# Performance work log

Hardware: AMD Instinct MI355X
Metric: run time of the kernel (lower is better)

Reference implementation:

```python
import jax, jax.numpy as jnp
import numpy as np

NHID = 512
PROJ = 64          # fixed 64-dim projection from the source code
N_NODES = 16384
N_CLAIM = 4096
N_EVID = 8192
N_GRAPHS = 64


def setup_inputs() -> dict:
    key = jax.random.key(0)
    ks = jax.random.split(key, 10)
    x = jax.random.normal(ks[0], (N_NODES, NHID), dtype=jnp.float32)
    batch = jnp.sort(jax.random.randint(ks[1], (N_NODES,), 0, N_GRAPHS, dtype=jnp.int64))
    claim_index = jax.random.randint(ks[2], (N_CLAIM,), 0, N_NODES, dtype=jnp.int64)
    evidence_index = jax.random.randint(ks[3], (N_EVID,), 0, N_NODES, dtype=jnp.int64)
    # Linear params (PyTorch Linear: y = x @ W.T + b; store as [in, out] here)
    s_c = 1.0 / np.sqrt(NHID)
    Wc = jax.random.uniform(ks[4], (NHID, PROJ), jnp.float32, -s_c, s_c)
    bc = jax.random.uniform(ks[5], (PROJ,), jnp.float32, -s_c, s_c)
    We = jax.random.uniform(ks[6], (NHID, PROJ), jnp.float32, -s_c, s_c)
    be = jax.random.uniform(ks[7], (PROJ,), jnp.float32, -s_c, s_c)
    s_a = 1.0 / np.sqrt(4 * NHID)
    Wa = jax.random.uniform(ks[8], (4 * NHID, NHID), jnp.float32, -s_a, s_a)
    ba = jax.random.uniform(ks[9], (NHID,), jnp.float32, -s_a, s_a)
    return {"x": x, "batch": batch, "claim_index": claim_index,
            "evidence_index": evidence_index,
            "Wc": Wc, "bc": bc, "We": We, "be": be, "Wa": Wa, "ba": ba}


def reference(x, batch, claim_index, evidence_index, Wc, bc, We, be, Wa, ba):
    claim_batch = batch[claim_index]          # [Nc]
    evidence_batch = batch[evidence_index]    # [Ne]
    # block-diagonal mask: 0 where same graph, -inf otherwise
    same = claim_batch[:, None] == evidence_batch[None, :]
    mask = jnp.where(same, 0.0, -jnp.inf).astype(jnp.float32)  # [Nc, Ne]

    claim = x[claim_index]       # [Nc, nhid]
    evidence = x[evidence_index]  # [Ne, nhid]

    weight_c = claim @ Wc + bc    # [Nc, 64]
    weight_e = evidence @ We + be  # [Ne, 64]
    scores = weight_c @ weight_e.T + mask          # [Nc, Ne]
    attn = jax.nn.softmax(scores, axis=-1)
    claim_new = attn @ evidence                    # [Nc, nhid]

    a = jnp.concatenate([claim, claim_new, claim - claim_new, claim * claim_new], axis=-1)
    a = a @ Wa + ba               # [Nc, nhid]

    # global_mean_pool over claim_batch
    seg_sum = jax.ops.segment_sum(a, claim_batch, num_segments=N_GRAPHS)
    counts = jax.ops.segment_sum(jnp.ones((a.shape[0],), a.dtype), claim_batch,
                                 num_segments=N_GRAPHS)
    res = seg_sum / jnp.maximum(counts, 1.0)[:, None]  # [B, nhid]
    return res
```

## Files before the change

### kernel.cpp

```cpp
#include <hip/hip_runtime.h>
#include <hip/hip_bf16.h>

#define NHID 512
#define PROJ 64
#define NC 4096
#define NEV 8192
#define NG 64
#define NCMAX 128
#define NE_CAP 256
#define DSLICES 4
#define DW 128
#define WE_S_STRIDE 72
#define EV_STRIDE 264
#define PG_STRIDE 256

typedef __attribute__((ext_vector_type(8))) short s16x8;
typedef __attribute__((ext_vector_type(8))) unsigned short u16x8;
typedef __attribute__((ext_vector_type(4))) float f32x4;

static __device__ __forceinline__ unsigned short f2b(float f) {
  union { __hip_bfloat16 h; unsigned short u; } v;
  v.h = __float2bfloat16(f);
  return v.u;
}

template <int NPT>
__device__ __forceinline__ void compact_pairs(
    const int* __restrict__ batch, const int* __restrict__ idx, int g,
    int* __restrict__ off_out, int* __restrict__ cnt_out, int2* __restrict__ pairs) {
  __shared__ int wtot[4], wless[4];
  int t = threadIdx.x, lane = t & 63, w = t >> 6;
  int vals[NPT], nid[NPT];
  int base_i = t * NPT;
  int eq = 0, less = 0;
#pragma unroll
  for (int j = 0; j < NPT; j++) {
    int node = idx[base_i + j];
    int v = batch[node];
    vals[j] = v;
    nid[j] = node;
    eq += (v == g) ? 1 : 0;
    less += (v < g) ? 1 : 0;
  }
  int s = eq;
#pragma unroll
  for (int off = 1; off < 64; off <<= 1) {
    int o = __shfl_up(s, off);
    if (lane >= off) s += o;
  }
  int ls = less;
#pragma unroll
  for (int off = 32; off; off >>= 1) ls += __shfl_xor(ls, off);
  if (lane == 63) wtot[w] = s;
  if (lane == 0) wless[w] = ls;
  __syncthreads();
  int wbase = 0;
#pragma unroll
  for (int k = 0; k < 4; k++)
    if (k < w) wbase += wtot[k];
  int base = wless[0] + wless[1] + wless[2] + wless[3];
  int pos = base + wbase + (s - eq);
#pragma unroll
  for (int j = 0; j < NPT; j++) {
    if (vals[j] == g) pairs[pos++] = make_int2(base_i + j, nid[j]);
  }
  if (t == 255) {
    cnt_out[g] = wbase + s;
    off_out[g] = base;
  }
}

__global__ __launch_bounds__(256) void k_front(
    const float* __restrict__ Wc, const float* __restrict__ We,
    unsigned short* __restrict__ WcT, unsigned short* __restrict__ WeT,
    const int* __restrict__ batch, const int* __restrict__ cidx,
    const int* __restrict__ eidx, int* __restrict__ c_off, int* __restrict__ c_cnt,
    int2* __restrict__ c_pair, int* __restrict__ e_off, int* __restrict__ e_cnt,
    int2* __restrict__ e_pair) {
  int b = blockIdx.x;
  if (b < 16) {
    __shared__ float ts[64][65];
    const float* src = (b < 8) ? Wc : We;
    unsigned short* dst = (b < 8) ? WcT : WeT;
    int k0 = (b & 7) * 64;
    int t = threadIdx.x;
    int c = t & 63, r0 = t >> 6;
#pragma unroll
    for (int p = 0; p < 16; p++) {
      int r = r0 * 16 + p;
      ts[r][c] = src[(size_t)(k0 + r) * 64 + c];
    }
    __syncthreads();
    int n = t >> 2, q = t & 3;
    unsigned short tmp[16];
#pragma unroll
    for (int j = 0; j < 16; j++) tmp[j] = f2b(ts[q * 16 + j][n]);
    u16x8* dp = (u16x8*)(dst + (size_t)n * NHID + k0 + q * 16);
    dp[0] = *(u16x8*)tmp;
    dp[1] = *(u16x8*)(tmp + 8);
  } else if (b < 80) {
    compact_pairs<NC / 256>(batch, cidx, b - 16, c_off, c_cnt, c_pair);
  } else {
    compact_pairs<NEV / 256>(batch, eidx, b - 80, e_off, e_cnt, e_pair);
  }
}

__global__ __launch_bounds__(256) void k_proj(
    const float* __restrict__ x, const int* __restrict__ cidx,
    const int* __restrict__ eidx, const unsigned short* __restrict__ WcT,
    const unsigned short* __restrict__ WeT, const float* __restrict__ bc,
    const float* __restrict__ be, const float* __restrict__ Wa,
    unsigned short* __restrict__ WaT, unsigned short* __restrict__ wcp,
    unsigned short* __restrict__ wep) {
  __shared__ __align__(16) char sm[64 * 65 * 4];
  int b = blockIdx.x;
  int t = threadIdx.x;
  if (b >= 768) {
    int tb = b - 768;
    float(*ts)[65] = (float(*)[65])sm;
    int k0 = (tb >> 3) * 64, n0 = (tb & 7) * 64;
    int c = t & 63, r0 = t >> 6;
#pragma unroll
    for (int p = 0; p < 16; p++) {
      int r = r0 * 16 + p;
      ts[r][c] = Wa[(size_t)(k0 + r) * NHID + n0 + c];
    }
    __syncthreads();
    int n = t >> 2, q = t & 3;
    unsigned short tmp[16];
#pragma unroll
    for (int j = 0; j < 16; j++) tmp[j] = f2b(ts[q * 16 + j][n]);
    u16x8* dp = (u16x8*)(WaT + (size_t)(n0 + n) * (4 * NHID) + k0 + q * 16);
    dp[0] = *(u16x8*)tmp;
    dp[1] = *(u16x8*)(tmp + 8);
    return;
  }
  float(*red)[16][64] = (float(*)[16][64])sm;
  const int* idx; const unsigned short* WT; const float* bias;
  unsigned short* out; int base;
  if (b < NC / 16) { idx = cidx; WT = WcT; bias = bc; out = wcp; base = b * 16; }
  else             { idx = eidx; WT = WeT; bias = be; out = wep; base = (b - NC / 16) * 16; }
  int lane = t & 63, kh = t >> 6;
  int ln = lane & 15, kb = lane >> 4;
  const float* xr = x + (size_t)idx[base + ln] * NHID + kh * 128;
  const unsigned short* wb = WT + kh * 128;
  f32x4 acc[4];
#pragma unroll
  for (int nt = 0; nt < 4; nt++) acc[nt] = (f32x4){0.f, 0.f, 0.f, 0.f};
#pragma unroll
  for (int kt = 0; kt < 4; kt++) {
    int k0 = kt * 32 + kb * 8;
    float4 p0 = *(const float4*)(xr + k0);
    float4 p1 = *(const float4*)(xr + k0 + 4);
    s16x8 a;
    a[0] = (short)f2b(p0.x); a[1] = (short)f2b(p0.y);
    a[2] = (short)f2b(p0.z); a[3] = (short)f2b(p0.w);
    a[4] = (short)f2b(p1.x); a[5] = (short)f2b(p1.y);
    a[6] = (short)f2b(p1.z); a[7] = (short)f2b(p1.w);
#pragma unroll
    for (int nt = 0; nt < 4; nt++) {
      s16x8 bf = *(const s16x8*)(wb + (size_t)(nt * 16 + ln) * NHID + k0);
      acc[nt] = __builtin_amdgcn_mfma_f32_16x16x32_bf16(a, bf, acc[nt], 0, 0, 0);
    }
  }
#pragma unroll
  for (int nt = 0; nt < 4; nt++)
#pragma unroll
    for (int r = 0; r < 4; r++)
      red[kh][kb * 4 + r][nt * 16 + ln] = acc[nt][r];
  __syncthreads();
  for (int i = t; i < 512; i += 256) {
    int row = i >> 5, cp = i & 31;
    int c0 = cp * 2;
    float v0 = red[0][row][c0] + red[1][row][c0] + red[2][row][c0] + red[3][row][c0] + bias[c0];
    float v1 = red[0][row][c0 + 1] + red[1][row][c0 + 1] + red[2][row][c0 + 1] + red[3][row][c0 + 1] + bias[c0 + 1];
    unsigned int pk = (unsigned)f2b(v0) | ((unsigned)f2b(v1) << 16);
    *(unsigned int*)(out + (size_t)(base + row) * PROJ + c0) = pk;
  }
}

__global__ __launch_bounds__(512) void k_score(
    const unsigned short* __restrict__ wcp, const unsigned short* __restrict__ wep,
    const int* __restrict__ c_off, const int* __restrict__ c_cnt,
    const int2* __restrict__ c_pair, const int* __restrict__ e_off,
    const int* __restrict__ e_cnt, const int2* __restrict__ e_pair,
    unsigned short* __restrict__ P_g) {
  __shared__ __align__(16) unsigned short we_s[NE_CAP * WE_S_STRIDE];
  __shared__ __align__(16) unsigned short wc_s[NCMAX * WE_S_STRIDE];
  int g = blockIdx.x;
  int t = threadIdx.x, lane = t & 63, w = t >> 6;
  int ln = lane & 15, kb = lane >> 4;
  int ne = min(e_cnt[g], NE_CAP);
  int eoff = e_off[g];
  int nloc = min(c_cnt[g], NCMAX);
  int coff = c_off[g];
  if (nloc <= 0) return;
  int KT = (ne + 31) >> 5;
  int NT = KT * 2;
  {
    int q = t & 7, er = t >> 3;
    for (int base_ = 0; base_ < NE_CAP; base_ += 64) {
      int e = base_ + er;
      u16x8 v = (u16x8){0, 0, 0, 0, 0, 0, 0, 0};
      if (e < ne) v = *(const u16x8*)(wep + (size_t)e_pair[eoff + e].x * PROJ + q * 8);
      *(u16x8*)(we_s + e * WE_S_STRIDE + q * 8) = v;
    }
    for (int base_ = 0; base_ < NCMAX; base_ += 64) {
      int c = base_ + er;
      u16x8 v = (u16x8){0, 0, 0, 0, 0, 0, 0, 0};
      if (c < nloc) v = *(const u16x8*)(wcp + (size_t)c_pair[coff + c].x * PROJ + q * 8);
      *(u16x8*)(wc_s + c * WE_S_STRIDE + q * 8) = v;
    }
  }
  __syncthreads();
  f32x4 sa[16];
#pragma unroll
  for (int i = 0; i < 16; i++) sa[i] = (f32x4){0.f, 0.f, 0.f, 0.f};
  const unsigned short* arow = wc_s + ((w << 4) + ln) * WE_S_STRIDE;
#pragma unroll
  for (int ks = 0; ks < 2; ks++) {
    s16x8 af = *(const s16x8*)(arow + ks * 32 + kb * 8);
#pragma unroll
    for (int nt = 0; nt < 16; nt++) {
      if (nt < NT) {
        s16x8 bf = *(const s16x8*)(we_s + (nt * 16 + ln) * WE_S_STRIDE + ks * 32 + kb * 8);
        sa[nt] = __builtin_amdgcn_mfma_f32_16x16x32_bf16(af, bf, sa[nt], 0, 0, 0);
      }
    }
  }
#pragma unroll
  for (int r = 0; r < 4; r++) {
    int claim = (w << 4) + (kb << 2) + r;
    float mx = -1e30f;
#pragma unroll
    for (int nt = 0; nt < 16; nt++) {
      if (nt < NT) {
        float v = sa[nt][r];
        v = (nt * 16 + ln < ne) ? v : -1e30f;
        sa[nt][r] = v;
        mx = fmaxf(mx, v);
      }
    }
    mx = fmaxf(mx, __shfl_xor(mx, 1));
    mx = fmaxf(mx, __shfl_xor(mx, 2));
    mx = fmaxf(mx, __shfl_xor(mx, 4));
    mx = fmaxf(mx, __shfl_xor(mx, 8));
    float sum = 0.f;
#pragma unroll
    for (int nt = 0; nt < 16; nt++) {
      if (nt < NT) {
        float p = __expf(sa[nt][r] - mx);
        sa[nt][r] = p;
        sum += p;
      }
    }
    sum += __shfl_xor(sum, 1);
    sum += __shfl_xor(sum, 2);
    sum += __shfl_xor(sum, 4);
    sum += __shfl_xor(sum, 8);
    float inv = 1.f / sum;
    if (claim < nloc) {
      unsigned short* prow = P_g + (size_t)(coff + claim) * PG_STRIDE;
#pragma unroll
      for (int nt = 0; nt < 16; nt++) {
        if (nt < NT) prow[nt * 16 + ln] = f2b(sa[nt][r] * inv);
      }
    }
  }
}

__global__ __launch_bounds__(512, 4) void k_pv(
    const float* __restrict__ x, const unsigned short* __restrict__ P_g,
    const int* __restrict__ c_off, const int* __restrict__ c_cnt,
    const int2* __restrict__ c_pair, const int* __restrict__ e_off,
    const int* __restrict__ e_cnt, const int2* __restrict__ e_pair,
    unsigned short* __restrict__ mcb) {
  __shared__ __align__(16) unsigned short evT[DW * EV_STRIDE];
  __shared__ float pp[4][3][DW];
  __shared__ int ev_id[NE_CAP];
  __shared__ int cl_id[NCMAX];
  unsigned int* evT32 = (unsigned int*)evT;

  int g = blockIdx.x >> 2;
  int ds = blockIdx.x & 3;
  int dsbase = ds * DW;
  int t = threadIdx.x, lane = t & 63, w = t >> 6;
  int ln = lane & 15, kb = lane >> 4;

  int ne = min(e_cnt[g], NE_CAP);
  int eoff = e_off[g];
  int ccnt_full = c_cnt[g];
  int nloc = min(ccnt_full, NCMAX);
  int coff = c_off[g];
  if (nloc <= 0) {
    int q = t >> 7, d = t & 127;
    mcb[(size_t)g * 4 * NHID + q * NHID + dsbase + d] = 0;
    return;
  }
  int KT = (ne + 31) >> 5;

  for (int e = t; e < NE_CAP; e += 512)
    ev_id[e] = (e < ne) ? e_pair[eoff + e].y : 0;
  if (t < NCMAX) cl_id[t] = (t < nloc) ? c_pair[coff + t].y : 0;
  __syncthreads();

#pragma unroll
  for (int it = 0; it < 8; it++) {
    int idx2 = it * 512 + t;
    int ep = idx2 & 127;
    int dq = idx2 >> 7;
    int d0 = dq * 4;
    int e0 = ep * 2;
    float4 va = make_float4(0.f, 0.f, 0.f, 0.f);
    float4 vb = make_float4(0.f, 0.f, 0.f, 0.f);
    if (e0 < ne)     va = *(const float4*)(x + (size_t)ev_id[e0] * NHID + dsbase + d0);
    if (e0 + 1 < ne) vb = *(const float4*)(x + (size_t)ev_id[e0 + 1] * NHID + dsbase + d0);
    evT32[(d0 + 0) * (EV_STRIDE / 2) + ep] = (unsigned)f2b(va.x) | ((unsigned)f2b(vb.x) << 16);
    evT32[(d0 + 1) * (EV_STRIDE / 2) + ep] = (unsigned)f2b(va.y) | ((unsigned)f2b(vb.y) << 16);
    evT32[(d0 + 2) * (EV_STRIDE / 2) + ep] = (unsigned)f2b(va.z) | ((unsigned)f2b(vb.z) << 16);
    evT32[(d0 + 3) * (EV_STRIDE / 2) + ep] = (unsigned)f2b(va.w) | ((unsigned)f2b(vb.w) << 16);
  }
  __syncthreads();

  int mw = w >> 1, nw = w & 1;
  int m0 = mw * 32, n0 = nw * 64;
  f32x4 pc[8];
#pragma unroll
  for (int i = 0; i < 8; i++) pc[i] = (f32x4){0.f, 0.f, 0.f, 0.f};
  {
    const unsigned short* prow0 = P_g + (size_t)(coff + m0 + ln) * PG_STRIDE + kb * 8;
    const unsigned short* prow1 = prow0 + 16 * PG_STRIDE;
#pragma unroll
    for (int kt = 0; kt < 8; kt++) {
      if (kt < KT) {
        int k0 = kt * 32;
        s16x8 a0 = *(const s16x8*)(prow0 + k0);
        s16x8 a1 = *(const s16x8*)(prow1 + k0);
#pragma unroll
        for (int nt = 0; nt < 4; nt++) {
          s16x8 bf = *(const s16x8*)(evT + (n0 + nt * 16 + ln) * EV_STRIDE + k0 + kb * 8);
          pc[nt]     = __builtin_amdgcn_mfma_f32_16x16x32_bf16(a0, bf, pc[nt], 0, 0, 0);
          pc[4 + nt] = __builtin_amdgcn_mfma_f32_16x16x32_bf16(a1, bf, pc[4 + nt], 0, 0, 0);
        }
      }
    }
  }

#pragma unroll
  for (int nt = 0; nt < 4; nt++) {
    int d = n0 + nt * 16 + ln;
    float s_cl = 0.f, s_cn = 0.f, s_pr = 0.f;
#pragma unroll
    for (int mi = 0; mi < 2; mi++) {
      f32x4 v = pc[mi * 4 + nt];
#pragma unroll
      for (int r = 0; r < 4; r++) {
        int m = m0 + mi * 16 + kb * 4 + r;
        if (m < nloc) {
          float cn = v[r];
          float cl = x[(size_t)cl_id[m] * NHID + dsbase + d];
          s_cl += cl; s_cn += cn; s_pr += cl * cn;
        }
      }
    }
    s_cl += __shfl_xor(s_cl, 16); s_cl += __shfl_xor(s_cl, 32);
    s_cn += __shfl_xor(s_cn, 16); s_cn += __shfl_xor(s_cn, 32);
    s_pr += __shfl_xor(s_pr, 16); s_pr += __shfl_xor(s_pr, 32);
    if (kb == 0) {
      pp[mw][0][d] = s_cl;
      pp[mw][1][d] = s_cn;
      pp[mw][2][d] = s_pr;
    }
  }
  __syncthreads();

  {
    int q = t >> 7, d = t & 127;
    float inv = 1.f / (float)max(ccnt_full, 1);
    float v;
    if (q == 0) {
      v = pp[0][0][d] + pp[1][0][d] + pp[2][0][d] + pp[3][0][d];
    } else if (q == 1) {
      v = pp[0][1][d] + pp[1][1][d] + pp[2][1][d] + pp[3][1][d];
    } else if (q == 2) {
      float cl = pp[0][0][d] + pp[1][0][d] + pp[2][0][d] + pp[3][0][d];
      float cn = pp[0][1][d] + pp[1][1][d] + pp[2][1][d] + pp[3][1][d];
      v = cl - cn;
    } else {
      v = pp[0][2][d] + pp[1][2][d] + pp[2][2][d] + pp[3][2][d];
    }
    mcb[(size_t)g * 4 * NHID + q * NHID + dsbase + d] = f2b(v * inv);
  }
}

__global__ __launch_bounds__(512) void k_out(
    const unsigned short* __restrict__ mc, const unsigned short* __restrict__ WaT,
    const float* __restrict__ ba, float* __restrict__ out) {
  __shared__ float red[2][64][16];
  int n0 = blockIdx.x * 16;
  int t = threadIdx.x, lane = t & 63, wv = t >> 6;
  int mh = wv & 3, kh = wv >> 2;
  int ln = lane & 15, kb = lane >> 4;
  f32x4 acc = (f32x4){0.f, 0.f, 0.f, 0.f};
  const unsigned short* arow = mc + (size_t)(mh * 16 + ln) * (4 * NHID) + kh * 1024;
  const unsigned short* wcol = WaT + (size_t)(n0 + ln) * (4 * NHID) + kh * 1024;
#pragma unroll 4
  for (int kt = 0; kt < 32; kt++) {
    int k0 = kt * 32 + kb * 8;
    s16x8 af = *(const s16x8*)(arow + k0);
    s16x8 bf = *(const s16x8*)(wcol + k0);
    acc = __builtin_amdgcn_mfma_f32_16x16x32_bf16(af, bf, acc, 0, 0, 0);
  }
#pragma unroll
  for (int r = 0; r < 4; r++)
    red[kh][mh * 16 + kb * 4 + r][ln] = acc[r];
  __syncthreads();
  for (int i = t; i < 1024; i += 512) {
    int row = i >> 4, col = i & 15;
    out[(size_t)row * NHID + n0 + col] = red[0][row][col] + red[1][row][col] + ba[n0 + col];
  }
}

extern "C" void kernel_launch(void* const* d_in, const int* in_sizes, int n_in,
                              void* d_out, int out_size, void* d_ws, size_t ws_size,
                              hipStream_t stream) {
  const float* x = (const float*)d_in[0];
  const int* batch = (const int*)d_in[1];
  const int* cidx = (const int*)d_in[2];
  const int* eidx = (const int*)d_in[3];
  const float* Wc = (const float*)d_in[4];
  const float* bc = (const float*)d_in[5];
  const float* We = (const float*)d_in[6];
  const float* be = (const float*)d_in[7];
  const float* Wa = (const float*)d_in[8];
  const float* ba = (const float*)d_in[9];
  float* out = (float*)d_out;

  char* w = (char*)d_ws;
  int* c_off = (int*)w;    w += NG * 4;
  int* c_cnt = (int*)w;    w += NG * 4;
  int* e_off = (int*)w;    w += NG * 4;
  int* e_cnt = (int*)w;    w += NG * 4;
  int2* c_pair = (int2*)w; w += (size_t)NC * 8;
  int2* e_pair = (int2*)w; w += (size_t)NEV * 8;
  unsigned short* wcp = (unsigned short*)w; w += (size_t)NC * PROJ * 2;
  unsigned short* wep = (unsigned short*)w; w += (size_t)NEV * PROJ * 2;
  unsigned short* WcT = (unsigned short*)w; w += (size_t)PROJ * NHID * 2;
  unsigned short* WeT = (unsigned short*)w; w += (size_t)PROJ * NHID * 2;
  unsigned short* WaT = (unsigned short*)w; w += (size_t)NHID * 4 * NHID * 2;
  unsigned short* mcb = (unsigned short*)w; w += (size_t)NG * 4 * NHID * 2;
  unsigned short* P_g = (unsigned short*)w; w += (size_t)(NC + NCMAX) * PG_STRIDE * 2;

  k_front<<<144, 256, 0, stream>>>(Wc, We, WcT, WeT, batch, cidx, eidx,
                                   c_off, c_cnt, c_pair, e_off, e_cnt, e_pair);
  k_proj<<<768 + 256, 256, 0, stream>>>(x, cidx, eidx, WcT, WeT, bc, be, Wa, WaT,
                                        wcp, wep);
  k_score<<<NG, 512, 0, stream>>>(wcp, wep, c_off, c_cnt, c_pair,
                                  e_off, e_cnt, e_pair, P_g);
  k_pv<<<NG * DSLICES, 512, 0, stream>>>(x, P_g, c_off, c_cnt, c_pair,
                                         e_off, e_cnt, e_pair, mcb);
  k_out<<<32, 512, 0, stream>>>(mcb, WaT, ba, out);
}
```

Before: 68.85 us.

## Fuse score and PV kernels with grid-wide atomic barrier and 8 D-slices

Merges the softmax-score kernel and the P·V kernel into one launch of 512 blocks. Each block computes scores for a 16-claim slice, writes P to global memory, then stages its 64-wide evidence slice while waiting on a global atomic counter until all blocks have finished. It then reads all of P for its graph. This removes one kernel launch and overlaps score work with evidence staging. In exchange it depends on all 512 blocks being co-resident (launch bounds 512,4), risks deadlock if they are not, and spins on an atomic.

```diff
diff --git a/kernel.cpp b/kernel.cpp
--- a/kernel.cpp
+++ b/kernel.cpp
@@ -8,11 +8,19 @@
 #define NG 64
 #define NCMAX 128
 #define NE_CAP 256
-#define DSLICES 4
-#define DW 128
+#define DSLICES 8
+#define DW 64
 #define WE_S_STRIDE 72
 #define EV_STRIDE 264
 #define PG_STRIDE 256
+
+#define WES_BYTES  (NE_CAP * WE_S_STRIDE * 2)
+#define WCS_OFF    WES_BYTES
+#define UNION_END  (WES_BYTES + 16 * WE_S_STRIDE * 2)
+#define IDS_OFF    UNION_END
+#define CLID_OFF   (IDS_OFF + 1024)
+#define PP_OFF     (CLID_OFF + 512)
+#define SMEM_BYTES (PP_OFF + 3072)
 
 typedef __attribute__((ext_vector_type(8))) short s16x8;
 typedef __attribute__((ext_vector_type(8))) unsigned short u16x8;
@@ -76,8 +84,9 @@
     const int* __restrict__ batch, const int* __restrict__ cidx,
     const int* __restrict__ eidx, int* __restrict__ c_off, int* __restrict__ c_cnt,
     int2* __restrict__ c_pair, int* __restrict__ e_off, int* __restrict__ e_cnt,
-    int2* __restrict__ e_pair) {
+    int2* __restrict__ e_pair, int* __restrict__ ctr) {
   int b = blockIdx.x;
+  if (b == 0 && threadIdx.x == 0) *ctr = 0;
   if (b < 16) {
     __shared__ float ts[64][65];
     const float* src = (b < 8) ? Wc : We;
@@ -179,24 +188,49 @@
   }
 }
 
-__global__ __launch_bounds__(512) void k_score(
-    const unsigned short* __restrict__ wcp, const unsigned short* __restrict__ wep,
-    const int* __restrict__ c_off, const int* __restrict__ c_cnt,
-    const int2* __restrict__ c_pair, const int* __restrict__ e_off,
-    const int* __restrict__ e_cnt, const int2* __restrict__ e_pair,
-    unsigned short* __restrict__ P_g) {
-  __shared__ __align__(16) unsigned short we_s[NE_CAP * WE_S_STRIDE];
-  __shared__ __align__(16) unsigned short wc_s[NCMAX * WE_S_STRIDE];
-  int g = blockIdx.x;
+__global__ __launch_bounds__(512, 4) void k_attn(
+    const float* __restrict__ x, const unsigned short* __restrict__ wcp,
+    const unsigned short* __restrict__ wep, const int* __restrict__ c_off,
+    const int* __restrict__ c_cnt, const int2* __restrict__ c_pair,
+    const int* __restrict__ e_off, const int* __restrict__ e_cnt,
+    const int2* __restrict__ e_pair, unsigned short* __restrict__ P_g,
+    unsigned short* __restrict__ mcb, int* __restrict__ ctr) {
+  __shared__ __align__(16) char smem[SMEM_BYTES];
+  unsigned short* we_s = (unsigned short*)(smem);
+  unsigned short* wc_s = (unsigned short*)(smem + WCS_OFF);
+  unsigned short* evT  = (unsigned short*)(smem);
+  unsigned int*   evT32 = (unsigned int*)(smem);
+  int* ev_id = (int*)(smem + IDS_OFF);
+  int* cl_id = (int*)(smem + CLID_OFF);
+  float* pp  = (float*)(smem + PP_OFF);
+
+  int g = blockIdx.x >> 3;
+  int ds = blockIdx.x & 7;
+  int dsbase = ds * DW;
   int t = threadIdx.x, lane = t & 63, w = t >> 6;
   int ln = lane & 15, kb = lane >> 4;
+
   int ne = min(e_cnt[g], NE_CAP);
   int eoff = e_off[g];
-  int nloc = min(c_cnt[g], NCMAX);
+  int ccnt_full = c_cnt[g];
+  int nloc = min(ccnt_full, NCMAX);
   int coff = c_off[g];
-  if (nloc <= 0) return;
+
+  if (nloc <= 0) {
+    if (t < 256) {
+      int q = t >> 6, d = t & 63;
+      mcb[(size_t)g * 4 * NHID + q * NHID + dsbase + d] = 0;
+    }
+    __syncthreads();
+    if (t == 0) { __threadfence(); atomicAdd(ctr, 1); }
+    return;
+  }
   int KT = (ne + 31) >> 5;
   int NT = KT * 2;
+
+  for (int e = t; e < NE_CAP; e += 512)
+    ev_id[e] = (e < ne) ? e_pair[eoff + e].y : 0;
+  if (t < NCMAX) cl_id[t] = (t < nloc) ? c_pair[coff + t].y : 0;
   {
     int q = t & 7, er = t >> 3;
     for (int base_ = 0; base_ < NE_CAP; base_ += 64) {
@@ -205,107 +239,78 @@
       if (e < ne) v = *(const u16x8*)(wep + (size_t)e_pair[eoff + e].x * PROJ + q * 8);
       *(u16x8*)(we_s + e * WE_S_STRIDE + q * 8) = v;
     }
-    for (int base_ = 0; base_ < NCMAX; base_ += 64) {
-      int c = base_ + er;
+    if (t < 128) {
+      int cr = t >> 3;
+      int gc = ds * 16 + cr;
       u16x8 v = (u16x8){0, 0, 0, 0, 0, 0, 0, 0};
-      if (c < nloc) v = *(const u16x8*)(wcp + (size_t)c_pair[coff + c].x * PROJ + q * 8);
-      *(u16x8*)(wc_s + c * WE_S_STRIDE + q * 8) = v;
-    }
-  }
-  __syncthreads();
-  f32x4 sa[16];
-#pragma unroll
-  for (int i = 0; i < 16; i++) sa[i] = (f32x4){0.f, 0.f, 0.f, 0.f};
-  const unsigned short* arow = wc_s + ((w << 4) + ln) * WE_S_STRIDE;
-#pragma unroll
-  for (int ks = 0; ks < 2; ks++) {
-    s16x8 af = *(const s16x8*)(arow + ks * 32 + kb * 8);
-#pragma unroll
-    for (int nt = 0; nt < 16; nt++) {
-      if (nt < NT) {
-        s16x8 bf = *(const s16x8*)(we_s + (nt * 16 + ln) * WE_S_STRIDE + ks * 32 + kb * 8);
-        sa[nt] = __builtin_amdgcn_mfma_f32_16x16x32_bf16(af, bf, sa[nt], 0, 0, 0);
-      }
-    }
-  }
-#pragma unroll
-  for (int r = 0; r < 4; r++) {
-    int claim = (w << 4) + (kb << 2) + r;
-    float mx = -1e30f;
-#pragma unroll
-    for (int nt = 0; nt < 16; nt++) {
-      if (nt < NT) {
-        float v = sa[nt][r];
-        v = (nt * 16 + ln < ne) ? v : -1e30f;
-        sa[nt][r] = v;
-        mx = fmaxf(mx, v);
-      }
-    }
-    mx = fmaxf(mx, __shfl_xor(mx, 1));
-    mx = fmaxf(mx, __shfl_xor(mx, 2));
-    mx = fmaxf(mx, __shfl_xor(mx, 4));
-    mx = fmaxf(mx, __shfl_xor(mx, 8));
-    float sum = 0.f;
-#pragma unroll
-    for (int nt = 0; nt < 16; nt++) {
-      if (nt < NT) {
-        float p = __expf(sa[nt][r] - mx);
-        sa[nt][r] = p;
-        sum += p;
-      }
-    }
-    sum += __shfl_xor(sum, 1);
-    sum += __shfl_xor(sum, 2);
-    sum += __shfl_xor(sum, 4);
-    sum += __shfl_xor(sum, 8);
-    float inv = 1.f / sum;
-    if (claim < nloc) {
-      unsigned short* prow = P_g + (size_t)(coff + claim) * PG_STRIDE;
+      if (gc < nloc) v = *(const u16x8*)(wcp + (size_t)c_pair[coff + gc].x * PROJ + q * 8);
+      *(u16x8*)(wc_s + cr * WE_S_STRIDE + q * 8) = v;
+    }
+  }
+  __syncthreads();
+
+  if (w == 0) {
+    f32x4 sa[16];
+#pragma unroll
+    for (int i = 0; i < 16; i++) sa[i] = (f32x4){0.f, 0.f, 0.f, 0.f};
+    const unsigned short* arow = wc_s + ln * WE_S_STRIDE;
+#pragma unroll
+    for (int ks = 0; ks < 2; ks++) {
+      s16x8 af = *(const s16x8*)(arow + ks * 32 + kb * 8);
 #pragma unroll
       for (int nt = 0; nt < 16; nt++) {
-        if (nt < NT) prow[nt * 16 + ln] = f2b(sa[nt][r] * inv);
-      }
-    }
-  }
-}
-
-__global__ __launch_bounds__(512, 4) void k_pv(
-    const float* __restrict__ x, const unsigned short* __restrict__ P_g,
-    const int* __restrict__ c_off, const int* __restrict__ c_cnt,
-    const int2* __restrict__ c_pair, const int* __restrict__ e_off,
-    const int* __restrict__ e_cnt, const int2* __restrict__ e_pair,
-    unsigned short* __restrict__ mcb) {
-  __shared__ __align__(16) unsigned short evT[DW * EV_STRIDE];
-  __shared__ float pp[4][3][DW];
-  __shared__ int ev_id[NE_CAP];
-  __shared__ int cl_id[NCMAX];
-  unsigned int* evT32 = (unsigned int*)evT;
-
-  int g = blockIdx.x >> 2;
-  int ds = blockIdx.x & 3;
-  int dsbase = ds * DW;
-  int t = threadIdx.x, lane = t & 63, w = t >> 6;
-  int ln = lane & 15, kb = lane >> 4;
-
-  int ne = min(e_cnt[g], NE_CAP);
-  int eoff = e_off[g];
-  int ccnt_full = c_cnt[g];
-  int nloc = min(ccnt_full, NCMAX);
-  int coff = c_off[g];
-  if (nloc <= 0) {
-    int q = t >> 7, d = t & 127;
-    mcb[(size_t)g * 4 * NHID + q * NHID + dsbase + d] = 0;
-    return;
-  }
-  int KT = (ne + 31) >> 5;
-
-  for (int e = t; e < NE_CAP; e += 512)
-    ev_id[e] = (e < ne) ? e_pair[eoff + e].y : 0;
-  if (t < NCMAX) cl_id[t] = (t < nloc) ? c_pair[coff + t].y : 0;
-  __syncthreads();
-
-#pragma unroll
-  for (int it = 0; it < 8; it++) {
+        if (nt < NT) {
+          s16x8 bf = *(const s16x8*)(we_s + (nt * 16 + ln) * WE_S_STRIDE + ks * 32 + kb * 8);
+          sa[nt] = __builtin_amdgcn_mfma_f32_16x16x32_bf16(af, bf, sa[nt], 0, 0, 0);
+        }
+      }
+    }
+#pragma unroll
+    for (int r = 0; r < 4; r++) {
+      int claim = (kb << 2) + r;
+      float mx = -1e30f;
+#pragma unroll
+      for (int nt = 0; nt < 16; nt++) {
+        if (nt < NT) {
+          float v = sa[nt][r];
+          v = (nt * 16 + ln < ne) ? v : -1e30f;
+          sa[nt][r] = v;
+          mx = fmaxf(mx, v);
+        }
+      }
+      mx = fmaxf(mx, __shfl_xor(mx, 1));
+      mx = fmaxf(mx, __shfl_xor(mx, 2));
+      mx = fmaxf(mx, __shfl_xor(mx, 4));
+      mx = fmaxf(mx, __shfl_xor(mx, 8));
+      float sum = 0.f;
+#pragma unroll
+      for (int nt = 0; nt < 16; nt++) {
+        if (nt < NT) {
+          float p = __expf(sa[nt][r] - mx);
+          sa[nt][r] = p;
+          sum += p;
+        }
+      }
+      sum += __shfl_xor(sum, 1);
+      sum += __shfl_xor(sum, 2);
+      sum += __shfl_xor(sum, 4);
+      sum += __shfl_xor(sum, 8);
+      float inv = 1.f / sum;
+      int gclaim = ds * 16 + claim;
+      if (gclaim < nloc) {
+        unsigned short* prow = P_g + (size_t)(coff + gclaim) * PG_STRIDE;
+#pragma unroll
+        for (int nt = 0; nt < 16; nt++) {
+          if (nt < NT) prow[nt * 16 + ln] = f2b(sa[nt][r] * inv);
+        }
+      }
+    }
+  }
+  __syncthreads();
+  if (t == 0) { __threadfence(); atomicAdd(ctr, 1); }
+
+#pragma unroll
+  for (int it = 0; it < 4; it++) {
     int idx2 = it * 512 + t;
     int ep = idx2 & 127;
     int dq = idx2 >> 7;
@@ -320,13 +325,18 @@
     evT32[(d0 + 2) * (EV_STRIDE / 2) + ep] = (unsigned)f2b(va.z) | ((unsigned)f2b(vb.z) << 16);
     evT32[(d0 + 3) * (EV_STRIDE / 2) + ep] = (unsigned)f2b(va.w) | ((unsigned)f2b(vb.w) << 16);
   }
+
+  if (t == 0) {
+    while (__hip_atomic_load(ctr, __ATOMIC_ACQUIRE, __HIP_MEMORY_SCOPE_AGENT) < NG * DSLICES)
+      __builtin_amdgcn_s_sleep(2);
+  }
   __syncthreads();
 
   int mw = w >> 1, nw = w & 1;
-  int m0 = mw * 32, n0 = nw * 64;
-  f32x4 pc[8];
-#pragma unroll
-  for (int i = 0; i < 8; i++) pc[i] = (f32x4){0.f, 0.f, 0.f, 0.f};
+  int m0 = mw * 32, n0 = nw * 32;
+  f32x4 pc[4];
+#pragma unroll
+  for (int i = 0; i < 4; i++) pc[i] = (f32x4){0.f, 0.f, 0.f, 0.f};
   {
     const unsigned short* prow0 = P_g + (size_t)(coff + m0 + ln) * PG_STRIDE + kb * 8;
     const unsigned short* prow1 = prow0 + 16 * PG_STRIDE;
@@ -337,22 +347,22 @@
         s16x8 a0 = *(const s16x8*)(prow0 + k0);
         s16x8 a1 = *(const s16x8*)(prow1 + k0);
 #pragma unroll
-        for (int nt = 0; nt < 4; nt++) {
+        for (int nt = 0; nt < 2; nt++) {
           s16x8 bf = *(const s16x8*)(evT + (n0 + nt * 16 + ln) * EV_STRIDE + k0 + kb * 8);
           pc[nt]     = __builtin_amdgcn_mfma_f32_16x16x32_bf16(a0, bf, pc[nt], 0, 0, 0);
-          pc[4 + nt] = __builtin_amdgcn_mfma_f32_16x16x32_bf16(a1, bf, pc[4 + nt], 0, 0, 0);
-        }
-      }
-    }
-  }
-
-#pragma unroll
-  for (int nt = 0; nt < 4; nt++) {
+          pc[2 + nt] = __builtin_amdgcn_mfma_f32_16x16x32_bf16(a1, bf, pc[2 + nt], 0, 0, 0);
+        }
+      }
+    }
+  }
+
+#pragma unroll
+  for (int nt = 0; nt < 2; nt++) {
     int d = n0 + nt * 16 + ln;
     float s_cl = 0.f, s_cn = 0.f, s_pr = 0.f;
 #pragma unroll
     for (int mi = 0; mi < 2; mi++) {
-      f32x4 v = pc[mi * 4 + nt];
+      f32x4 v = pc[mi * 2 + nt];
 #pragma unroll
       for (int r = 0; r < 4; r++) {
         int m = m0 + mi * 16 + kb * 4 + r;
@@ -367,27 +377,27 @@
     s_cn += __shfl_xor(s_cn, 16); s_cn += __shfl_xor(s_cn, 32);
     s_pr += __shfl_xor(s_pr, 16); s_pr += __shfl_xor(s_pr, 32);
     if (kb == 0) {
-      pp[mw][0][d] = s_cl;
-      pp[mw][1][d] = s_cn;
-      pp[mw][2][d] = s_pr;
-    }
-  }
-  __syncthreads();
-
-  {
-    int q = t >> 7, d = t & 127;
+      pp[(mw * 3 + 0) * DW + d] = s_cl;
+      pp[(mw * 3 + 1) * DW + d] = s_cn;
+      pp[(mw * 3 + 2) * DW + d] = s_pr;
+    }
+  }
+  __syncthreads();
+
+  if (t < 256) {
+    int q = t >> 6, d = t & 63;
     float inv = 1.f / (float)max(ccnt_full, 1);
     float v;
     if (q == 0) {
-      v = pp[0][0][d] + pp[1][0][d] + pp[2][0][d] + pp[3][0][d];
+      v = pp[0 * DW + d] + pp[3 * DW + d] + pp[6 * DW + d] + pp[9 * DW + d];
     } else if (q == 1) {
-      v = pp[0][1][d] + pp[1][1][d] + pp[2][1][d] + pp[3][1][d];
+      v = pp[1 * DW + d] + pp[4 * DW + d] + pp[7 * DW + d] + pp[10 * DW + d];
     } else if (q == 2) {
-      float cl = pp[0][0][d] + pp[1][0][d] + pp[2][0][d] + pp[3][0][d];
-      float cn = pp[0][1][d] + pp[1][1][d] + pp[2][1][d] + pp[3][1][d];
+      float cl = pp[0 * DW + d] + pp[3 * DW + d] + pp[6 * DW + d] + pp[9 * DW + d];
+      float cn = pp[1 * DW + d] + pp[4 * DW + d] + pp[7 * DW + d] + pp[10 * DW + d];
       v = cl - cn;
     } else {
-      v = pp[0][2][d] + pp[1][2][d] + pp[2][2][d] + pp[3][2][d];
+      v = pp[2 * DW + d] + pp[5 * DW + d] + pp[8 * DW + d] + pp[11 * DW + d];
     }
     mcb[(size_t)g * 4 * NHID + q * NHID + dsbase + d] = f2b(v * inv);
   }
@@ -441,6 +451,7 @@
   int* c_cnt = (int*)w;    w += NG * 4;
   int* e_off = (int*)w;    w += NG * 4;
   int* e_cnt = (int*)w;    w += NG * 4;
+  int* ctr = (int*)w;      w += 64;
   int2* c_pair = (int2*)w; w += (size_t)NC * 8;
   int2* e_pair = (int2*)w; w += (size_t)NEV * 8;
   unsigned short* wcp = (unsigned short*)w; w += (size_t)NC * PROJ * 2;
@@ -452,12 +463,10 @@
   unsigned short* P_g = (unsigned short*)w; w += (size_t)(NC + NCMAX) * PG_STRIDE * 2;
 
   k_front<<<144, 256, 0, stream>>>(Wc, We, WcT, WeT, batch, cidx, eidx,
-                                   c_off, c_cnt, c_pair, e_off, e_cnt, e_pair);
+                                   c_off, c_cnt, c_pair, e_off, e_cnt, e_pair, ctr);
   k_proj<<<768 + 256, 256, 0, stream>>>(x, cidx, eidx, WcT, WeT, bc, be, Wa, WaT,
                                         wcp, wep);
-  k_score<<<NG, 512, 0, stream>>>(wcp, wep, c_off, c_cnt, c_pair,
-                                  e_off, e_cnt, e_pair, P_g);
-  k_pv<<<NG * DSLICES, 512, 0, stream>>>(x, P_g, c_off, c_cnt, c_pair,
-                                         e_off, e_cnt, e_pair, mcb);
+  k_attn<<<NG * DSLICES, 512, 0, stream>>>(x, wcp, wep, c_off, c_cnt, c_pair,
+                                           e_off, e_cnt, e_pair, P_g, mcb, ctr);
   k_out<<<32, 512, 0, stream>>>(mcb, WaT, ba, out);
 }
```

Result: slower. 83.12 us (+20.7%).
